# Optimization experiments

Measured on AMD Instinct MI355X. Metric: run time of the kernel, lower is better.

The kernel has to match this reference:

```python
import jax, jax.numpy as jnp
import numpy as np

B, C, K, V, S = 16384, 1024, 128, 256, 6
HM, HG, M = 512, 384, 1024
LB = 2
GATE_DIM = C + K + 2 * V + 5  # 1669
CADENCE = 8.0
TEMP = 0.25
REFRESH_T, SPAWN_T, PROMOTE_T, RETIRE_T = 0.55, 0.60, 0.50, 0.15
DECAY = 0.995
EPS_N = 1e-6


def _mlp(x, W1, b1, W2, b2):
    return jax.nn.gelu(x @ W1 + b1, approximate=False) @ W2 + b2


def _l2norm(x):
    n = jnp.linalg.norm(x, axis=-1, keepdims=True)
    return x / jnp.maximum(n, EPS_N)


def setup_inputs():
    key = jax.random.key(0)
    ks = jax.random.split(key, 16)
    p = lambda k, sh: (0.02 * jax.random.normal(k, sh)).astype(jnp.float32)
    return {
        "context": jax.random.normal(ks[0], (B, C), jnp.float32),
        "ledger_bias": jax.random.normal(ks[1], (B, LB), jnp.float32),
        "keys": jax.random.normal(ks[2], (B, S, K), jnp.float32),
        "values": jax.random.normal(ks[3], (B, S, V), jnp.float32),
        "confidence": jax.random.uniform(ks[4], (B, S, 1), jnp.float32),
        "age": 16.0 * jax.random.uniform(ks[5], (B, S, 1), jnp.float32),
        "alive": (jax.random.uniform(ks[6], (B, S, 1)) > 0.3).astype(jnp.float32),
        "Wk1": p(ks[7], (C, HM)), "bk1": jnp.zeros(HM, jnp.float32),
        "Wk2": p(ks[8], (HM, K)), "bk2": jnp.zeros(K, jnp.float32),
        "Wv1": p(ks[9], (C, HM)), "bv1": jnp.zeros(HM, jnp.float32),
        "Wv2": p(ks[10], (HM, V)), "bv2": jnp.zeros(V, jnp.float32),
        "Wg1": p(ks[11], (4, GATE_DIM, HG)), "bg1": jnp.zeros((4, HG), jnp.float32),
        "Wg2": p(ks[12], (4, HG, 1)), "bg2": jnp.zeros((4, 1), jnp.float32),
        "Wsum": p(ks[13], (V, M)), "bsum": jnp.zeros(M, jnp.float32),
        "g_ln": jnp.ones(M, jnp.float32), "b_ln": jnp.zeros(M, jnp.float32),
    }


def _forward(context, ledger_bias, keys, values, confidence, age, alive,
             Wk1, bk1, Wk2, bk2, Wv1, bv1, Wv2, bv2,
             Wg1, bg1, Wg2, bg2, Wsum, bsum, g_ln, b_ln):
    cand_key = _l2norm(_mlp(context, Wk1, bk1, Wk2, bk2))   # [B,K]
    cand_val = _mlp(context, Wv1, bv1, Wv2, bv2)            # [B,V]
    # --- slot match: cosine similarity over live slots, gather best ---
    live = alive[..., 0] > 0                                # [B,S]
    safe_keys = _l2norm(keys + (1.0 - alive) * 1e-4)
    scores = jnp.einsum("bd,bsd->bs", cand_key, safe_keys)
    scores = jnp.where(live, scores, -1e4)
    has_live = jnp.any(live, axis=1, keepdims=True)         # [B,1]
    best_score = jnp.where(has_live, scores.max(axis=1, keepdims=True), 0.0)
    best_index = jnp.where(has_live, jnp.argmax(scores, axis=1, keepdims=True), 0)
    matched_val = jnp.take_along_axis(values, best_index[:, :, None], axis=1)[:, 0]
    matched_age = jnp.take_along_axis(age, best_index[:, :, None], axis=1)[:, 0]
    cadence_prior = jax.nn.sigmoid((matched_age - CADENCE) / CADENCE)
    surprise = 1.0 - best_score
    feats = jnp.concatenate([context, cand_key, cand_val, matched_val,
                             best_score, cadence_prior, surprise, ledger_bias], axis=-1)
    # --- four gate MLPs fused into one batched einsum ---
    h = jax.nn.gelu(jnp.einsum("bf,gfh->bgh", feats, Wg1) + bg1, approximate=False)
    probs = jax.nn.sigmoid(jnp.einsum("bgh,gho->bgo", h, Wg2) + bg2)[:, :, 0]  # [B,4]
    refresh_p, spawn_p, promote_p, retire_p = (probs[:, i:i + 1] for i in range(4))
    # --- soft masks (hard=False path) ---
    has_live_f = alive.max(axis=1)                          # [B,1]
    t = max(TEMP, 1e-4)
    refresh_raw = jax.nn.sigmoid((refresh_p - REFRESH_T) / t) * has_live_f
    spawn_raw = jax.nn.sigmoid((spawn_p - SPAWN_T) / t)
    denom = 1.0 + refresh_raw + spawn_raw
    refresh = refresh_raw / denom
    spawn = spawn_raw / denom
    promote = jax.nn.sigmoid((promote_p - PROMOTE_T) / t)
    retire = jax.nn.sigmoid((retire_p - RETIRE_T) / t)
    # --- spawn slot selection ---
    inactive = (alive[..., 0] < 0.5).astype(jnp.float32)
    has_inactive = inactive.max(axis=1, keepdims=True) > 0.5
    inactive_choice = jnp.argmax(inactive, axis=1, keepdims=True)
    utility = (confidence - 0.01 * age)[..., 0]
    utility = jnp.where(best_index == jnp.arange(S)[None, :], 1e4, utility)
    spawn_index = jnp.where(has_inactive, inactive_choice,
                            jnp.argmin(utility, axis=1, keepdims=True))
    # --- masked scatter update into slot memory ---
    match_hot = jax.nn.one_hot(best_index[:, 0], S, dtype=keys.dtype)[:, :, None]
    spawn_hot = jax.nn.one_hot(spawn_index[:, 0], S, dtype=keys.dtype)[:, :, None]
    refresh_slot = match_hot * refresh[:, None, :]
    spawn_slot = spawn_hot * spawn[:, None, :]
    retire_slot = match_hot * retire[:, None, :]
    write = jnp.clip(refresh_slot + spawn_slot, 0.0, 1.0)
    keys_n = keys * (1.0 - write) + write * cand_key[:, None, :]
    values_n = values * (1.0 - write) + write * cand_val[:, None, :]
    conf_n = (confidence * DECAY * (1.0 - write) + write) * (1.0 - retire_slot)
    age_n = (age + alive) * (1.0 - write)
    alive_n = jnp.clip(alive * (1.0 - retire_slot) + write, 0.0, 1.0)
    # --- confidence-weighted summary + promoted memory token ---
    w = alive_n * conf_n
    summary = (values_n * w).sum(axis=1) / (w.sum(axis=1) + EPS_N)  # [B,V]
    z = summary @ Wsum + bsum
    mu = z.mean(axis=-1, keepdims=True)
    var = ((z - mu) ** 2).mean(axis=-1, keepdims=True)
    promoted = promote * (((z - mu) / jnp.sqrt(var + 1e-5)) * g_ln + b_ln)
    return promoted, summary, keys_n, values_n, conf_n, age_n, alive_n


def reference(context, ledger_bias, keys, values, confidence, age, alive,
              Wk1, bk1, Wk2, bk2, Wv1, bv1, Wv2, bv2,
              Wg1, bg1, Wg2, bg2, Wsum, bsum, g_ln, b_ln):
    return _forward(context, ledger_bias, keys, values, confidence, age, alive,
                    Wk1, bk1, Wk2, bk2, Wv1, bv1, Wv2, bv2,
                    Wg1, bg1, Wg2, bg2, Wsum, bsum, g_ln, b_ln)
```

## Files before the change

kernel.cpp:

```cpp
#include <hip/hip_runtime.h>
#include <math.h>

static constexpr int Bsz  = 16384;
static constexpr int Cdim = 1024;
static constexpr int Kdim = 128;
static constexpr int Vdim = 256;
static constexpr int HMd  = 512;
static constexpr int GOUTd= 1536;
static constexpr int GDIM = 1669;
static constexpr int GPAD = 1728;
static constexpr int F2D  = 704;
static constexpr int Mdim = 1024;
static constexpr float TAU = 2e-3f;

typedef __attribute__((ext_vector_type(8))) _Float16 f16x8;
typedef __attribute__((ext_vector_type(4))) _Float16 f16x4;
typedef __attribute__((ext_vector_type(4))) float f32x4;

__device__ __forceinline__ float sigm(float x){ return 1.0f/(1.0f+__expf(-x)); }
__device__ __forceinline__ float gelu(float x){
    float y = 0.70710678118654752440f * x;
    float a = fabsf(y);
    float t1 = __builtin_amdgcn_rcpf(fmaf(0.3275911f, a, 1.0f));
    float p = t1*fmaf(t1, fmaf(t1, fmaf(t1, fmaf(t1, 1.061405429f, -1.453152027f),
                                         1.421413741f), -0.284496736f), 0.254829592f);
    float e = __expf(-a*a);
    float er = fmaf(-p, e, 1.0f);
    er = (y < 0.0f) ? -er : er;
    return 0.5f*x*(1.0f+er);
}
__device__ __forceinline__ ushort f2h(float f){
    return __builtin_bit_cast(ushort, (_Float16)f);
}
__device__ __forceinline__ unsigned f2q4(float a, float b, float c, float d){
    int v = 0;
    v = __builtin_amdgcn_cvt_pk_fp8_f32(a, b, v, false);
    v = __builtin_amdgcn_cvt_pk_fp8_f32(c, d, v, true);
    return (unsigned)v;
}


__global__ __launch_bounds__(256) void k_zero(int* p){ if (threadIdx.x==0) *p = 0; }

__global__ __launch_bounds__(256) void k_cat(float* __restrict__ dst,
        const float* __restrict__ a, const float* __restrict__ b, int na, int ntot){
    int i = blockIdx.x*256 + threadIdx.x;
    if (i >= ntot) return;
    dst[i] = (i < na) ? a[i] : b[i-na];
}

__global__ __launch_bounds__(256) void k_wt(const float* __restrict__ W,
                                            ushort* __restrict__ Wt, int K, int N){
    __shared__ float tile[64][65];
    int n0 = blockIdx.x*64, k0 = blockIdx.y*64;
    int tx = threadIdx.x & 63, ty = threadIdx.x >> 6;
    #pragma unroll
    for (int i=0;i<64;i+=4)
        tile[ty+i][tx] = W[(size_t)(k0+ty+i)*N + n0 + tx];
    __syncthreads();
    #pragma unroll
    for (int i=0;i<64;i+=4)
        Wt[(size_t)(n0+ty+i)*K + k0 + tx] = f2h(tile[tx][ty+i]);
}

__global__ __launch_bounds__(256) void k_wg1t8(const float* __restrict__ Wg1,
                                               unsigned char* __restrict__ B8){
    __shared__ float tile[64][65];
    int g  = blockIdx.z;
    int h0 = blockIdx.x*64;
    int f0 = blockIdx.y*64;
    int tx = threadIdx.x & 63, ty = threadIdx.x >> 6;
    #pragma unroll
    for (int i=0;i<64;i+=4)
        tile[ty+i][tx] = Wg1[((size_t)g*GDIM + f0+ty+i)*384 + h0+tx];
    __syncthreads();
    int u = threadIdx.x & 7, nl0 = threadIdx.x >> 3;
    #pragma unroll
    for (int i=0;i<2;i++){
        int nl = nl0 + i*32;
        float v[8];
        #pragma unroll
        for (int j=0;j<8;j++) v[j] = tile[u*8+j][nl];
        unsigned q0 = f2q4(v[0],v[1],v[2],v[3]), q1 = f2q4(v[4],v[5],v[6],v[7]);
        int n  = g*384 + h0 + nl;
        int ur = (f0>>3) + u;
        int seg = ur >> 4, ul = ur & 15;
        size_t pos = (size_t)n*1024 + seg*128 + (size_t)(ul ^ (n&7))*8;
        ((unsigned*)(B8+pos))[0] = q0;
        ((unsigned*)(B8+pos))[1] = q1;
    }
}

__global__ __launch_bounds__(256) void k_wg1tf(const float* __restrict__ Wg1,
                                               ushort* __restrict__ Wt){
    __shared__ float tile[64][65];
    int g  = blockIdx.z;
    int h0 = blockIdx.x*64;
    int k0 = blockIdx.y*64;
    int tx = threadIdx.x & 63, ty = threadIdx.x >> 6;
    #pragma unroll
    for (int i=0;i<64;i+=4){
        int f = 1024 + k0 + ty + i;
        tile[ty+i][tx] = (f < GDIM) ? Wg1[((size_t)g*GDIM + f)*384 + h0+tx] : 0.0f;
    }
    __syncthreads();
    #pragma unroll
    for (int i=0;i<64;i+=4)
        Wt[((size_t)(g*384 + h0+ty+i))*F2D + k0 + tx] = f2h(tile[tx][ty+i]);
}

__global__ __launch_bounds__(256) void k_cvt8(const float* __restrict__ x,
        ushort* __restrict__ yh, unsigned char* __restrict__ y8, int nunits){
    int i = blockIdx.x*256 + threadIdx.x;
    if (i >= nunits) return;
    const float4* src = (const float4*)(x + (size_t)i*8);
    float4 v0 = src[0], v1 = src[1];
    ushort4 h0 = { f2h(v0.x), f2h(v0.y), f2h(v0.z), f2h(v0.w) };
    ushort4 h1 = { f2h(v1.x), f2h(v1.y), f2h(v1.z), f2h(v1.w) };
    ((ushort4*)yh)[(size_t)i*2]   = h0;
    ((ushort4*)yh)[(size_t)i*2+1] = h1;
    unsigned q0 = f2q4(v0.x,v0.y,v0.z,v0.w), q1 = f2q4(v1.x,v1.y,v1.z,v1.w);
    int row = i >> 7;
    int ur  = i & 127;
    int seg = ur >> 4, ul = ur & 15;
    size_t pos = (size_t)row*1024 + seg*128 + (size_t)(ul ^ (row&7))*8;
    ((unsigned*)(y8+pos))[0] = q0;
    ((unsigned*)(y8+pos))[1] = q1;
}

__device__ __forceinline__ void gload_lds16(const void* g, void* l){
    typedef __attribute__((address_space(1))) const unsigned gu32;
    typedef __attribute__((address_space(3))) unsigned lu32;
    __builtin_amdgcn_global_load_lds((gu32*)(unsigned long long)g,
                                     (lu32*)(unsigned)(unsigned long long)l,
                                     16, 0, 0);
}

template<int ACT, int OUTM, int SRC, int NX>
__global__ __launch_bounds__(512, 4) void k_mgemm(const ushort* __restrict__ A,
        const ushort* __restrict__ A2, const ushort* __restrict__ Bt,
        const float* __restrict__ bias, const float* __restrict__ Wg2,
        void* __restrict__ Cout, int K, int lda){
    __shared__ alignas(16) ushort lds[24576];
    ushort* As = lds;
    ushort* Bs = lds + 16384;
    int t = threadIdx.x;
    int l = t & 63, wv = t >> 6;
    int wrow = wv >> 1, wcol = wv & 1;
    int nwg = NX * (int)gridDim.y;
    int orig = (int)blockIdx.y * NX + (int)blockIdx.x;
    int qq = nwg >> 3, rr = nwg & 7;
    int xcd = orig & 7, loc = orig >> 3;
    int wgid = (xcd < rr ? xcd*(qq+1) : rr*(qq+1) + (xcd-rr)*qq) + loc;
    int bx = wgid % NX;
    int by = wgid / NX;
    size_t row0 = (size_t)by * 256;
    int col0 = bx * 128;
    constexpr int N = NX*128;
    f32x4 acc[4][4] = {};
    int lrow = l >> 3;
    int lc8  = (l & 7) ^ lrow;

    for (int k0 = 0; k0 < K; k0 += 64){
        const ushort* Ag; size_t astr; int koff;
        if (SRC == 2){
            Ag = A; astr = (size_t)lda; koff = k0 + (bx ? 512 : 0);
        } else { Ag = A; astr = (size_t)lda; koff = k0; }
        #pragma unroll
        for (int i = 0; i < 4; ++i){
            int ch = wv*4 + i;
            int r  = ch*8 + lrow;
            gload_lds16(Ag + (row0 + r)*astr + koff + lc8*8, As + ch*512);
        }
        #pragma unroll
        for (int i = 0; i < 2; ++i){
            int ch = wv*2 + i;
            int r  = ch*8 + lrow;
            gload_lds16(Bt + (size_t)(col0 + r)*K + k0 + lc8*8, Bs + ch*512);
        }
        __syncthreads();
        #pragma unroll
        for (int kk = 0; kk < 2; ++kk){
            f16x8 af[4], bfr[4];
            int j8 = kk*4 + (l >> 4);
            #pragma unroll
            for (int m = 0; m < 4; ++m){
                int row = wrow*64 + m*16 + (l & 15);
                int c16 = j8 ^ (row & 7);
                af[m] = *(const f16x8*)(const void*)(As + row*64 + c16*8);
            }
            #pragma unroll
            for (int n = 0; n < 4; ++n){
                int rowb = wcol*64 + n*16 + (l & 15);
                int c16 = j8 ^ (rowb & 7);
                bfr[n] = *(const f16x8*)(const void*)(Bs + rowb*64 + c16*8);
            }
            #pragma unroll
            for (int m = 0; m < 4; ++m)
                #pragma unroll
                for (int n = 0; n < 4; ++n)
                    acc[m][n] = __builtin_amdgcn_mfma_f32_16x16x32_f16(af[m], bfr[n], acc[m][n], 0, 0, 0);
        }
        __syncthreads();
    }
    int q = l >> 4, cf = l & 15;
    #pragma unroll
    for (int m = 0; m < 4; ++m){
        #pragma unroll
        for (int n = 0; n < 4; ++n){
            int col = col0 + wcol*64 + n*16 + cf;
            float bv = bias[col];
            #pragma unroll
            for (int i = 0; i < 4; ++i){
                size_t r = row0 + wrow*64 + m*16 + q*4 + i;
                float v = acc[m][n][i] + bv;
                if (ACT == 1) v = gelu(v);
                if (OUTM == 1) ((ushort*)Cout)[r*N + col] = f2h(v);
                else           ((float*) Cout)[r*N + col] = v;
            }
        }
    }
}

__global__ __launch_bounds__(512, 4) void k_ggemm(const unsigned char* __restrict__ A8,
        const ushort* __restrict__ Af, const unsigned char* __restrict__ B8,
        const ushort* __restrict__ Bf, const float* __restrict__ bias,
        const float* __restrict__ Wg2, float* __restrict__ part){
    __shared__ alignas(16) unsigned char lds[49152];
    unsigned char* As8 = lds;
    unsigned char* Bs8 = lds + 32768;
    ushort* As16 = (ushort*)lds;
    ushort* Bs16 = (ushort*)(lds + 32768);
    int t = threadIdx.x, l = t & 63, wv = t >> 6;
    int wrow = wv >> 1, wcol = wv & 1;
    constexpr int NX = 12;
    int nwg = NX * (int)gridDim.y;
    int orig = (int)blockIdx.y * NX + (int)blockIdx.x;
    int qq = nwg >> 3, rr = nwg & 7;
    int xcd = orig & 7, loc = orig >> 3;
    int wgid = (xcd < rr ? xcd*(qq+1) : rr*(qq+1) + (xcd-rr)*qq) + loc;
    int bx = wgid % NX;
    int by = wgid / NX;
    size_t row0 = (size_t)by * 256;
    int col0 = bx * 128;
    f32x4 acc[4][4] = {};
    int lrow = l >> 3;

    for (int kt = 0; kt < 8; ++kt){
        int k0 = kt << 7;
        #pragma unroll
        for (int i = 0; i < 4; ++i){
            int ch = wv*4 + i;
            int r  = ch*8 + lrow;
            gload_lds16(A8 + (row0 + r)*1024 + k0 + (l&7)*16, As8 + ch*1024);
        }
        #pragma unroll
        for (int i = 0; i < 2; ++i){
            int ch = wv*2 + i;
            int r  = ch*8 + lrow;
            gload_lds16(B8 + (size_t)(col0 + r)*1024 + k0 + (l&7)*16, Bs8 + ch*1024);
        }
        __syncthreads();
        #pragma unroll
        for (int kk = 0; kk < 4; ++kk){
            long a8[4], b8[4];
            int j8 = (l >> 4) + kk*4;
            #pragma unroll
            for (int m = 0; m < 4; ++m){
                int row = wrow*64 + m*16 + (l & 15);
                int u = j8 ^ (row & 7);
                a8[m] = *(const long*)(const void*)(As8 + row*128 + u*8);
            }
            #pragma unroll
            for (int n = 0; n < 4; ++n){
                int col = wcol*64 + n*16 + (l & 15);
                int u = j8 ^ (col & 7);
                b8[n] = *(const long*)(const void*)(Bs8 + col*128 + u*8);
            }
            #pragma unroll
            for (int m = 0; m < 4; ++m)
                #pragma unroll
                for (int n = 0; n < 4; ++n)
                    acc[m][n] = __builtin_amdgcn_mfma_f32_16x16x32_fp8_fp8(a8[m], b8[n], acc[m][n], 0, 0, 0);
        }
        __syncthreads();
    }
    int lc8 = (l & 7) ^ lrow;
    for (int tt = 0; tt < 11; ++tt){
        int k0 = tt << 6;
        #pragma unroll
        for (int i = 0; i < 4; ++i){
            int ch = wv*4 + i;
            int r  = ch*8 + lrow;
            gload_lds16(Af + (row0 + r)*(size_t)F2D + k0 + lc8*8, As16 + ch*512);
        }
        #pragma unroll
        for (int i = 0; i < 2; ++i){
            int ch = wv*2 + i;
            int r  = ch*8 + lrow;
            gload_lds16(Bf + (size_t)(col0 + r)*F2D + k0 + lc8*8, Bs16 + ch*512);
        }
        __syncthreads();
        #pragma unroll
        for (int kk = 0; kk < 2; ++kk){
            f16x8 af[4], bfr[4];
            int j8 = kk*4 + (l >> 4);
            #pragma unroll
            for (int m = 0; m < 4; ++m){
                int row = wrow*64 + m*16 + (l & 15);
                int c16 = j8 ^ (row & 7);
                af[m] = *(const f16x8*)(const void*)(As16 + row*64 + c16*8);
            }
            #pragma unroll
            for (int n = 0; n < 4; ++n){
                int col = wcol*64 + n*16 + (l & 15);
                int c16 = j8 ^ (col & 7);
                bfr[n] = *(const f16x8*)(const void*)(Bs16 + col*64 + c16*8);
            }
            #pragma unroll
            for (int m = 0; m < 4; ++m)
                #pragma unroll
                for (int n = 0; n < 4; ++n)
                    acc[m][n] = __builtin_amdgcn_mfma_f32_16x16x32_f16(af[m], bfr[n], acc[m][n], 0, 0, 0);
        }
        __syncthreads();
    }
    int q = l >> 4, cf = l & 15;
    float* sacc = (float*)lds;
    if (t < 256) sacc[t] = 0.f;
    __syncthreads();
    #pragma unroll
    for (int m = 0; m < 4; ++m){
        #pragma unroll
        for (int i = 0; i < 4; ++i){
            float v = 0.f;
            #pragma unroll
            for (int n = 0; n < 4; ++n){
                int col = col0 + wcol*64 + n*16 + cf;
                float z = acc[m][n][i] + bias[col];
                v += gelu(z) * Wg2[col];
            }
            atomicAdd(&sacc[wrow*64 + m*16 + q*4 + i], v);
        }
    }
    __syncthreads();
    if (t < 256) part[(row0 + t)*NX + bx] = sacc[t];
}

template<int ACT, int GATHER>
__global__ __launch_bounds__(256) void k_gemm_dyn(const float* __restrict__ A,
                                                  const float* __restrict__ W,
                                                  const float* __restrict__ bias,
                                                  float* __restrict__ C,
                                                  const int* __restrict__ cntp,
                                                  const int* __restrict__ flaglist,
                                                  int b0, int N, int K){
    int cnt = *cntp;
    int M = (cnt + 63) & ~63;
    size_t row0 = (size_t)blockIdx.y * 64;
    if ((int)row0 >= M) return;
    __shared__ float As[32][68];
    __shared__ float Ws[32][64];
    int t  = threadIdx.x;
    int tx = t & 15, ty = t >> 4;
    int col0 = blockIdx.x * 64;
    float acc[4][4] = {};
    int ra = t >> 3;
    int ca = (t & 7) << 2;
    int rw = t >> 4;
    int cw = (t & 15) << 2;
    const float *Arow0, *Arow1;
    if (GATHER){
        int r1 = (int)row0 + ra, r2 = r1 + 32;
        int f1 = (r1 < cnt) ? flaglist[r1] : 0;
        int f2 = (r2 < cnt) ? flaglist[r2] : 0;
        Arow0 = A + ((size_t)b0 + f1)*K;
        Arow1 = A + ((size_t)b0 + f2)*K;
    } else {
        Arow0 = A + (row0 + ra)*(size_t)K;
        Arow1 = A + (row0 + ra + 32)*(size_t)K;
    }
    for (int k0 = 0; k0 < K; k0 += 32){
        float4 a0 = *(const float4*)(Arow0 + k0 + ca);
        float4 a1 = *(const float4*)(Arow1 + k0 + ca);
        float4 w0 = *(const float4*)(W + (size_t)(k0 + rw)*N + col0 + cw);
        float4 w1 = *(const float4*)(W + (size_t)(k0 + rw + 16)*N + col0 + cw);
        As[ca+0][ra] = a0.x; As[ca+1][ra] = a0.y; As[ca+2][ra] = a0.z; As[ca+3][ra] = a0.w;
        As[ca+0][ra+32] = a1.x; As[ca+1][ra+32] = a1.y; As[ca+2][ra+32] = a1.z; As[ca+3][ra+32] = a1.w;
        *(float4*)&Ws[rw][cw]    = w0;
        *(float4*)&Ws[rw+16][cw] = w1;
        __syncthreads();
        #pragma unroll
        for (int kk = 0; kk < 32; ++kk){
            float4 av = *(const float4*)&As[kk][ty*4];
            float4 wv = *(const float4*)&Ws[kk][tx*4];
            float a4[4] = {av.x, av.y, av.z, av.w};
            float w4[4] = {wv.x, wv.y, wv.z, wv.w};
            #pragma unroll
            for (int i=0;i<4;i++)
                #pragma unroll
                for (int j=0;j<4;j++)
                    acc[i][j] = fmaf(a4[i], w4[j], acc[i][j]);
        }
        __syncthreads();
    }
    #pragma unroll
    for (int i=0;i<4;i++){
        size_t r = row0 + ty*4 + i;
        #pragma unroll
        for (int j=0;j<4;j++){
            int c = col0 + tx*4 + j;
            float v = acc[i][j] + bias[c];
            if (ACT == 1) v = gelu(v);
            C[r*N + c] = v;
        }
    }
}

__global__ __launch_bounds__(256) void k_fixapply(const float* __restrict__ fck,
        const float* __restrict__ keys, const float* __restrict__ values,
        const float* __restrict__ age,  const float* __restrict__ alive,
        float* __restrict__ ckc, ushort* __restrict__ feats2, int* __restrict__ bidx,
        const int* __restrict__ flagcnt, const int* __restrict__ flaglist, int b0){
    int i = (blockIdx.x<<2) + (threadIdx.x>>6);
    int lane = threadIdx.x & 63;
    if (i >= *flagcnt) return;
    int w = flaglist[i];
    size_t b = (size_t)b0 + w;
    float2 c2 = ((const float2*)(fck + (size_t)i*128))[lane];
    float ss = c2.x*c2.x + c2.y*c2.y;
    #pragma unroll
    for (int o=32;o;o>>=1) ss += __shfl_xor(ss,o);
    float inv = 1.0f / fmaxf(sqrtf(ss), 1e-6f);
    float2 cc; cc.x = c2.x*inv; cc.y = c2.y*inv;
    ((float2*)(ckc + (size_t)w*128))[lane] = cc;
    ushort* f2 = feats2 + (size_t)w*F2D;
    { ushort2 o = { f2h(cc.x), f2h(cc.y) };
      ((ushort2*)f2)[lane] = o; }
    float s1v = -1e30f; int bi = 0; int anylive = 0;
    #pragma unroll
    for (int s=0;s<6;s++){
        float a = alive[b*6+s];
        float2 k2 = ((const float2*)(keys + (b*6+s)*128))[lane];
        float ks = k2.x*k2.x + k2.y*k2.y;
        float dt = cc.x*k2.x + cc.y*k2.y;
        #pragma unroll
        for (int o=32;o;o>>=1){ ks += __shfl_xor(ks,o); dt += __shfl_xor(dt,o); }
        float sc;
        if (a > 0.0f){ sc = dt / fmaxf(sqrtf(ks), 1e-6f); anylive = 1; }
        else sc = -1e4f;
        if (sc > s1v){ s1v = sc; bi = s; }
    }
    int bis = anylive ? bi : 0;
    float bsc = anylive ? s1v : 0.0f;
    float4 mv = ((const float4*)(values + (b*6+bis)*256))[lane];
    ushort4 mo = { f2h(mv.x), f2h(mv.y), f2h(mv.z), f2h(mv.w) };
    ((ushort4*)(f2+384))[lane] = mo;
    if (lane == 0){
        bidx[w] = bis;
        float mage = age[b*6 + bis];
        f2[640] = f2h(bsc);
        f2[641] = f2h(sigm((mage - 8.0f)*0.125f));
        f2[642] = f2h(1.0f - bsc);
    }
}

__global__ __launch_bounds__(256) void k_feats(
        const float* __restrict__ ledger, const float* __restrict__ keys,
        const float* __restrict__ values, const float* __restrict__ age,
        const float* __restrict__ alive,  const float* __restrict__ ckv,
        float* __restrict__ ckc, ushort* __restrict__ feats2,
        int* __restrict__ bidx, int* __restrict__ flagcnt, int* __restrict__ flaglist,
        int b0){
    int w = (blockIdx.x<<2) + (threadIdx.x>>6);
    int lane = threadIdx.x & 63;
    size_t b = (size_t)b0 + w;
    const float* ckr = ckv + (size_t)w*384;
    float2 cr2 = ((const float2*)ckr)[lane];
    float ssc = cr2.x*cr2.x + cr2.y*cr2.y;
    #pragma unroll
    for (int o=32;o;o>>=1) ssc += __shfl_xor(ssc,o);
    float invc = 1.0f / fmaxf(sqrtf(ssc), 1e-6f);
    float2 cc; cc.x = cr2.x*invc; cc.y = cr2.y*invc;
    ((float2*)(ckc + (size_t)w*128))[lane] = cc;
    float s1v = -1e30f, s2v = -1e30f; int bi = 0; int anylive = 0;
    #pragma unroll
    for (int s=0;s<6;s++){
        float a = alive[b*6+s];
        float2 k2 = ((const float2*)(keys + (b*6+s)*128))[lane];
        float ss = k2.x*k2.x + k2.y*k2.y;
        float dt = cc.x*k2.x + cc.y*k2.y;
        #pragma unroll
        for (int o=32;o;o>>=1){ ss += __shfl_xor(ss,o); dt += __shfl_xor(dt,o); }
        float sc;
        if (a > 0.0f){ sc = dt / fmaxf(sqrtf(ss), 1e-6f); anylive = 1; }
        else sc = -1e4f;
        if (sc > s1v){ s2v = s1v; s1v = sc; bi = s; }
        else if (sc > s2v) s2v = sc;
    }
    float best_score = anylive ? s1v : 0.0f;
    int bis = anylive ? bi : 0;
    if (lane == 0 && (s1v - s2v) < TAU){
        int pos = atomicAdd(flagcnt, 1);
        flaglist[pos] = w;
    }
    float4 mv = ((const float4*)(values + (b*6+bis)*256))[lane];
    float mage = age[b*6+bis];
    float cad = sigm((mage - 8.0f)*0.125f);
    ushort* f2 = feats2 + (size_t)w*F2D;
    { ushort2 o = { f2h(cc.x), f2h(cc.y) };
      ((ushort2*)f2)[lane] = o; }
    { float4 v = ((const float4*)(ckr+128))[lane];
      ushort4 o = { f2h(v.x), f2h(v.y), f2h(v.z), f2h(v.w) };
      ((ushort4*)(f2+128))[lane] = o; }
    { ushort4 o = { f2h(mv.x), f2h(mv.y), f2h(mv.z), f2h(mv.w) };
      ((ushort4*)(f2+384))[lane] = o; }
    if (lane == 0){
        f2[640] = f2h(best_score);
        f2[641] = f2h(cad);
        f2[642] = f2h(1.0f - best_score);
        f2[643] = f2h(ledger[b*2]);
        f2[644] = f2h(ledger[b*2+1]);
        bidx[w] = bis;
    }
    if (lane < GPAD - GDIM) f2[645+lane] = 0;
}

__global__ __launch_bounds__(256) void k_update(const float* __restrict__ keys,
        const float* __restrict__ values, const float* __restrict__ conf,
        const float* __restrict__ age,    const float* __restrict__ alive,
        const float* __restrict__ ckC,    const float* __restrict__ ckv,
        const float* __restrict__ part,   const float* __restrict__ bg2,
        const int* __restrict__ bidx,
        float* __restrict__ probsC,
        float* __restrict__ o_keys, float* __restrict__ o_vals,
        float* __restrict__ o_conf, float* __restrict__ o_age,
        float* __restrict__ o_aliv, float* __restrict__ o_sum,
        ushort* __restrict__ o_sumb, int b0){
    int w = (blockIdx.x<<2) + (threadIdx.x>>6);
    int lane = threadIdx.x & 63;
    size_t b = (size_t)b0 + w;
    const float* pp = part + (size_t)w*12;
    float pb[4];
    #pragma unroll
    for (int g=0; g<4; ++g)
        pb[g] = sigm(pp[3*g] + pp[3*g+1] + pp[3*g+2] + bg2[g]);
    if (lane < 4) probsC[w*4 + lane] = pb[lane];
    float rp = pb[0], sp = pb[1], tp = pb[3];
    float al[6], cf[6], ag[6];
    float hl = 0.f;
    #pragma unroll
    for (int s=0;s<6;s++){
        al[s]=alive[b*6+s]; cf[s]=conf[b*6+s]; ag[s]=age[b*6+s];
        hl = fmaxf(hl, al[s]);
    }
    float rr = hl * sigm((rp-0.55f)*4.0f);
    float sr = sigm((sp-0.60f)*4.0f);
    float den = 1.0f + rr + sr;
    float refresh = rr/den, spawn = sr/den;
    float retire = sigm((tp-0.15f)*4.0f);
    int bi = bidx[w];
    int ic = -1;
    #pragma unroll
    for (int s=5;s>=0;s--) if (al[s] < 0.5f) ic = s;
    int si;
    if (ic >= 0) si = ic;
    else {
        float bu = 1e30f; int am = 0;
        #pragma unroll
        for (int s=0;s<6;s++){
            float u = (s == bi) ? 1e4f : (cf[s] - 0.01f*ag[s]);
            if (u < bu){ bu = u; am = s; }
        }
        si = am;
    }
    float2 cc  = ((const float2*)(ckC + (size_t)w*128))[lane];
    float4 cvv = ((const float4*)(ckv + (size_t)w*384 + 128))[lane];
    float s0=0,s1=0,s2=0,s3=0, wsum=0;
    #pragma unroll
    for (int s=0;s<6;s++){
        float wr = refresh*(s==bi ? 1.0f:0.0f) + spawn*(s==si ? 1.0f:0.0f);
        wr = fminf(wr, 1.0f);
        float rs = (s==bi) ? retire : 0.0f;
        float om = 1.0f - wr;
        float2 k2 = ((const float2*)(keys + (b*6+s)*128))[lane];
        float2 kn; kn.x = k2.x*om + wr*cc.x; kn.y = k2.y*om + wr*cc.y;
        ((float2*)(o_keys + (b*6+s)*128))[lane] = kn;
        float4 vv = ((const float4*)(values + (b*6+s)*256))[lane];
        float4 vn;
        vn.x = vv.x*om + wr*cvv.x; vn.y = vv.y*om + wr*cvv.y;
        vn.z = vv.z*om + wr*cvv.z; vn.w = vv.w*om + wr*cvv.w;
        ((float4*)(o_vals + (b*6+s)*256))[lane] = vn;
        float cn  = (cf[s]*0.995f*om + wr) * (1.0f - rs);
        float an  = fminf(fmaxf(al[s]*(1.0f - rs) + wr, 0.0f), 1.0f);
        float agn = (ag[s] + al[s]) * om;
        float wgt = an * cn;
        wsum += wgt;
        s0 += vn.x*wgt; s1 += vn.y*wgt; s2 += vn.z*wgt; s3 += vn.w*wgt;
        if (lane == s){ o_conf[b*6+s] = cn; o_age[b*6+s] = agn; o_aliv[b*6+s] = an; }
    }
    float inv = 1.0f/(wsum + 1e-6f);
    float4 sm; sm.x = s0*inv; sm.y = s1*inv; sm.z = s2*inv; sm.w = s3*inv;
    ((float4*)(o_sum + b*256))[lane] = sm;
    ushort4 sb = { f2h(sm.x), f2h(sm.y), f2h(sm.z), f2h(sm.w) };
    ((ushort4*)(o_sumb + (size_t)w*256))[lane] = sb;
}

__global__ __launch_bounds__(256) void k_ln(const ushort* __restrict__ z,
        const float* __restrict__ probs, const float* __restrict__ g_ln,
        const float* __restrict__ b_ln,  float* __restrict__ o_prom, int b0){
    int w = blockIdx.x; int t = threadIdx.x;
    int lane = t & 63, wid = t >> 6;
    f16x4 hv = ((const f16x4*)(z + (size_t)w*1024))[t];
    float v0 = (float)hv[0], v1 = (float)hv[1], v2 = (float)hv[2], v3 = (float)hv[3];
    float s = v0+v1+v2+v3;
    #pragma unroll
    for (int o=32;o;o>>=1) s += __shfl_xor(s,o);
    __shared__ float red[4];
    if (lane==0) red[wid] = s;
    __syncthreads();
    float mu = (red[0]+red[1]+red[2]+red[3]) * (1.0f/1024.0f);
    float d0=v0-mu, d1=v1-mu, d2=v2-mu, d3=v3-mu;
    float ss = d0*d0+d1*d1+d2*d2+d3*d3;
    #pragma unroll
    for (int o=32;o;o>>=1) ss += __shfl_xor(ss,o);
    __syncthreads();
    if (lane==0) red[wid] = ss;
    __syncthreads();
    float var = (red[0]+red[1]+red[2]+red[3]) * (1.0f/1024.0f);
    float rstd = 1.0f / sqrtf(var + 1e-5f);
    float pm = sigm((probs[w*4+2]-0.50f)*4.0f);
    float4 g  = ((const float4*)g_ln)[t];
    float4 bb = ((const float4*)b_ln)[t];
    float4 o;
    o.x = pm*(d0*rstd*g.x + bb.x);
    o.y = pm*(d1*rstd*g.y + bb.y);
    o.z = pm*(d2*rstd*g.z + bb.z);
    o.w = pm*(d3*rstd*g.w + bb.w);
    ((float4*)(o_prom + ((size_t)b0 + w)*1024))[t] = o;
}

extern "C" void kernel_launch(void* const* d_in, const int* in_sizes, int n_in,
                              void* d_out, int out_size, void* d_ws, size_t ws_size,
                              hipStream_t stream){
    const float* ctx    = (const float*)d_in[0];
    const float* ledger = (const float*)d_in[1];
    const float* keys   = (const float*)d_in[2];
    const float* values = (const float*)d_in[3];
    const float* conf   = (const float*)d_in[4];
    const float* age    = (const float*)d_in[5];
    const float* alive  = (const float*)d_in[6];
    const float* Wk1 = (const float*)d_in[7];  const float* bk1 = (const float*)d_in[8];
    const float* Wk2 = (const float*)d_in[9];  const float* bk2 = (const float*)d_in[10];
    const float* Wv1 = (const float*)d_in[11]; const float* bv1 = (const float*)d_in[12];
    const float* Wv2 = (const float*)d_in[13]; const float* bv2 = (const float*)d_in[14];
    const float* Wg1 = (const float*)d_in[15]; const float* bg1 = (const float*)d_in[16];
    const float* Wg2 = (const float*)d_in[17]; const float* bg2 = (const float*)d_in[18];
    const float* Wsum= (const float*)d_in[19]; const float* bsum= (const float*)d_in[20];
    const float* g_ln= (const float*)d_in[21]; const float* b_ln= (const float*)d_in[22];

    float* out   = (float*)d_out;
    float* o_prom= out;
    float* o_sum = o_prom + (size_t)Bsz*Mdim;
    float* o_keys= o_sum  + (size_t)Bsz*Vdim;
    float* o_vals= o_keys + (size_t)Bsz*6*Kdim;
    float* o_conf= o_vals + (size_t)Bsz*6*Vdim;
    float* o_age = o_conf + (size_t)Bsz*6;
    float* o_aliv= o_age  + (size_t)Bsz*6;

    char* p = (char*)d_ws;
    auto alloc = [&](size_t bytes)->char*{
        char* r = p; p += (bytes + 255) & ~(size_t)255; return r;
    };
    ushort* ctxh  = (ushort*)alloc((size_t)Bsz*Cdim*2);
    unsigned char* ctx8 = (unsigned char*)alloc((size_t)Bsz*Cdim);
    ushort* W1m   = (ushort*)alloc((size_t)1024*Cdim*2);
    ushort* W2m   = (ushort*)alloc((size_t)384*HMd*2);
    unsigned char* Wg1t8 = (unsigned char*)alloc((size_t)GOUTd*1024);
    ushort* Wg1tf = (ushort*)alloc((size_t)GOUTd*F2D*2);
    ushort* Wsumt = (ushort*)alloc((size_t)Mdim*Vdim*2);
    float*  biasm1= (float*) alloc(1024*4);
    float*  biasm2= (float*) alloc(384*4);
    size_t fixed = (size_t)(p - (char*)d_ws);
    size_t per_row = 2048 + 1536 + 512 + 1408 + 48 + 4096 + 512 + 16
                   + 4 + 4 + 2048 + 512 + 128;
    int CB = 16384;
    while (CB > 256 && fixed + (size_t)CB*per_row + 16384 > ws_size) CB >>= 1;
    ushort* H      = (ushort*)alloc((size_t)CB*1024*2);
    float*  ckv    = (float*) alloc((size_t)CB*384*4);
    float*  ckc    = (float*) alloc((size_t)CB*Kdim*4);
    ushort* feats2 = (ushort*)alloc((size_t)CB*F2D*2);
    float*  part   = (float*) alloc((size_t)CB*12*4);
    float*  zbuf   = (float*) alloc((size_t)CB*Mdim*4);
    ushort* sumb   = (ushort*)alloc((size_t)CB*Vdim*2);
    float*  probsC = (float*) alloc((size_t)CB*4*4);
    int*    bidxC  = (int*)   alloc((size_t)CB*4);
    int*    flagl  = (int*)   alloc((size_t)CB*4);
    int*    flagc  = (int*)   alloc(256);
    float*  fH     = (float*) alloc((size_t)CB*HMd*4);
    float*  fck    = (float*) alloc((size_t)CB*Kdim*4);
    ushort* zh     = (ushort*)zbuf;

    dim3 blk(256);
    dim3 blk512(512);
    k_cvt8<<<(int)(((size_t)Bsz*Cdim/8 + 255)/256), blk, 0, stream>>>(
        ctx, ctxh, ctx8, (int)((size_t)Bsz*Cdim/8));
    k_wt<<<dim3(HMd/64,  Cdim/64), blk, 0, stream>>>(Wk1, W1m,             Cdim, HMd);
    k_wt<<<dim3(HMd/64,  Cdim/64), blk, 0, stream>>>(Wv1, W1m + 512*Cdim,  Cdim, HMd);
    k_wt<<<dim3(Kdim/64, HMd/64),  blk, 0, stream>>>(Wk2, W2m,             HMd, Kdim);
    k_wt<<<dim3(Vdim/64, HMd/64),  blk, 0, stream>>>(Wv2, W2m + 128*HMd,   HMd, Vdim);
    k_wt<<<dim3(Mdim/64, Vdim/64), blk, 0, stream>>>(Wsum, Wsumt, Vdim, Mdim);
    k_wg1t8<<<dim3(6, 16, 4), blk, 0, stream>>>(Wg1, Wg1t8);
    k_wg1tf<<<dim3(6, 11, 4), blk, 0, stream>>>(Wg1, Wg1tf);
    k_cat<<<(1024+255)/256, blk, 0, stream>>>(biasm1, bk1, bv1, 512, 1024);
    k_cat<<<(384+255)/256,  blk, 0, stream>>>(biasm2, bk2, bv2, 128, 384);

    for (int b0 = 0; b0 < Bsz; b0 += CB){
        k_zero<<<1, blk, 0, stream>>>(flagc);
        k_mgemm<1,1,0,8><<<dim3(8, CB/256), blk512, 0, stream>>>(
            ctxh + (size_t)b0*Cdim, nullptr, W1m, biasm1, nullptr, H, Cdim, Cdim);
        k_mgemm<0,0,2,3><<<dim3(3, CB/256), blk512, 0, stream>>>(
            H, nullptr, W2m, biasm2, nullptr, ckv, HMd, 1024);
        k_feats<<<CB/4, blk, 0, stream>>>(ledger, keys, values, age, alive,
                                          ckv, ckc, feats2, bidxC, flagc, flagl, b0);
        k_gemm_dyn<1,1><<<dim3(HMd/64,  CB/64), blk, 0, stream>>>(
            ctx, Wk1, bk1, fH, flagc, flagl, b0, HMd, Cdim);
        k_gemm_dyn<0,0><<<dim3(Kdim/64, CB/64), blk, 0, stream>>>(
            fH, Wk2, bk2, fck, flagc, nullptr, 0, Kdim, HMd);
        k_fixapply<<<CB/4, blk, 0, stream>>>(fck, keys, values, age, alive,
                                             ckc, feats2, bidxC, flagc, flagl, b0);
        k_ggemm<<<dim3(12, CB/256), blk512, 0, stream>>>(
            ctx8 + (size_t)b0*Cdim, feats2, Wg1t8, Wg1tf, bg1, Wg2, part);
        k_update<<<CB/4, blk, 0, stream>>>(keys, values, conf, age, alive, ckc, ckv,
                                           part, bg2, bidxC, probsC,
                                           o_keys, o_vals, o_conf, o_age, o_aliv,
                                           o_sum, sumb, b0);
        k_mgemm<0,1,0,8><<<dim3(8, CB/256), blk512, 0, stream>>>(
            sumb, nullptr, Wsumt, bsum, nullptr, zh, Vdim, Vdim);
        k_ln<<<CB, blk, 0, stream>>>(zh, probsC, g_ln, b_ln, o_prom, b0);
    }
}
```

Measured before the change: 444.3 us.

## Quantize gate feature tail to FP8 and fold into single FP8 GEMM loop

The gate GEMM's second phase, which multiplied the 704-wide feature tail in FP16 MFMA, is replaced by FP8. A new kernel converts the FP16 features to swizzled FP8 rows, and the weight tail is pre-quantized the same way, so one 14-step FP8 loop covers both the context and the feature parts. Separately, the dynamic fixup GEMMs now use a fixed grid of 16 row blocks that stride over the flagged rows instead of launching CB/64 blocks that mostly exit early. This trades an extra conversion pass and lower precision on the gate features for halved operand bytes and faster MFMA in the tail.

New measurement: 455.9 us. +2.6%, slower.

```diff
diff --git a/kernel.cpp b/kernel.cpp
--- a/kernel.cpp
+++ b/kernel.cpp
@@ -8,8 +8,9 @@
 static constexpr int HMd  = 512;
 static constexpr int GOUTd= 1536;
 static constexpr int GDIM = 1669;
-static constexpr int GPAD = 1728;
+static constexpr int GPAD = 1792;
 static constexpr int F2D  = 704;
+static constexpr int F8D  = 768;
 static constexpr int Mdim = 1024;
 static constexpr float TAU = 2e-3f;
 
@@ -91,8 +92,8 @@
     }
 }
 
-__global__ __launch_bounds__(256) void k_wg1tf(const float* __restrict__ Wg1,
-                                               ushort* __restrict__ Wt){
+__global__ __launch_bounds__(256) void k_wg1tf8(const float* __restrict__ Wg1,
+                                                unsigned char* __restrict__ B8){
     __shared__ float tile[64][65];
     int g  = blockIdx.z;
     int h0 = blockIdx.x*64;
@@ -104,9 +105,21 @@
         tile[ty+i][tx] = (f < GDIM) ? Wg1[((size_t)g*GDIM + f)*384 + h0+tx] : 0.0f;
     }
     __syncthreads();
-    #pragma unroll
-    for (int i=0;i<64;i+=4)
-        Wt[((size_t)(g*384 + h0+ty+i))*F2D + k0 + tx] = f2h(tile[tx][ty+i]);
+    int u = threadIdx.x & 7, nl0 = threadIdx.x >> 3;
+    #pragma unroll
+    for (int i=0;i<2;i++){
+        int nl = nl0 + i*32;
+        float v[8];
+        #pragma unroll
+        for (int j=0;j<8;j++) v[j] = tile[u*8+j][nl];
+        unsigned q0 = f2q4(v[0],v[1],v[2],v[3]), q1 = f2q4(v[4],v[5],v[6],v[7]);
+        int n  = g*384 + h0 + nl;
+        int ur = (k0>>3) + u;
+        int seg = ur >> 4, ul = ur & 15;
+        size_t pos = (size_t)n*F8D + seg*128 + (size_t)(ul ^ (n&7))*8;
+        ((unsigned*)(B8+pos))[0] = q0;
+        ((unsigned*)(B8+pos))[1] = q1;
+    }
 }
 
 __global__ __launch_bounds__(256) void k_cvt8(const float* __restrict__ x,
@@ -126,6 +139,25 @@
     size_t pos = (size_t)row*1024 + seg*128 + (size_t)(ul ^ (row&7))*8;
     ((unsigned*)(y8+pos))[0] = q0;
     ((unsigned*)(y8+pos))[1] = q1;
+}
+
+__global__ __launch_bounds__(256) void k_f2q8(const ushort* __restrict__ f16,
+        unsigned char* __restrict__ f8, int total){
+    int idx = blockIdx.x*256 + threadIdx.x;
+    if (idx >= total) return;
+    int w = idx / 96, ur = idx - w*96;
+    int c0 = ur*8;
+    float v[8];
+    #pragma unroll
+    for (int j=0;j<8;j++){
+        int c = c0+j;
+        v[j] = (c < F2D) ? (float)(*(const _Float16*)&f16[(size_t)w*F2D + c]) : 0.0f;
+    }
+    unsigned q0 = f2q4(v[0],v[1],v[2],v[3]), q1 = f2q4(v[4],v[5],v[6],v[7]);
+    int seg = ur >> 4, ul = ur & 15;
+    size_t pos = (size_t)w*F8D + seg*128 + (size_t)(ul ^ (w&7))*8;
+    ((unsigned*)(f8+pos))[0] = q0;
+    ((unsigned*)(f8+pos))[1] = q1;
 }
 
 __device__ __forceinline__ void gload_lds16(const void* g, void* l){
@@ -223,14 +255,12 @@
 }
 
 __global__ __launch_bounds__(512, 4) void k_ggemm(const unsigned char* __restrict__ A8,
-        const ushort* __restrict__ Af, const unsigned char* __restrict__ B8,
-        const ushort* __restrict__ Bf, const float* __restrict__ bias,
+        const unsigned char* __restrict__ F8, const unsigned char* __restrict__ B8,
+        const unsigned char* __restrict__ BF8, const float* __restrict__ bias,
         const float* __restrict__ Wg2, float* __restrict__ part){
     __shared__ alignas(16) unsigned char lds[49152];
     unsigned char* As8 = lds;
     unsigned char* Bs8 = lds + 32768;
-    ushort* As16 = (ushort*)lds;
-    ushort* Bs16 = (ushort*)(lds + 32768);
     int t = threadIdx.x, l = t & 63, wv = t >> 6;
     int wrow = wv >> 1, wcol = wv & 1;
     constexpr int NX = 12;
@@ -246,24 +276,26 @@
     f32x4 acc[4][4] = {};
     int lrow = l >> 3;
 
-    for (int kt = 0; kt < 8; ++kt){
-        int k0 = kt << 7;
+    for (int kt = 0; kt < 14; ++kt){
+        const unsigned char *Ab, *Bb; size_t astr; int koff;
+        if (kt < 8){ Ab = A8; Bb = B8;  astr = 1024; koff = kt << 7; }
+        else       { Ab = F8; Bb = BF8; astr = F8D;  koff = (kt-8) << 7; }
         #pragma unroll
         for (int i = 0; i < 4; ++i){
             int ch = wv*4 + i;
             int r  = ch*8 + lrow;
-            gload_lds16(A8 + (row0 + r)*1024 + k0 + (l&7)*16, As8 + ch*1024);
+            gload_lds16(Ab + (row0 + r)*astr + koff + (l&7)*16, As8 + ch*1024);
         }
         #pragma unroll
         for (int i = 0; i < 2; ++i){
             int ch = wv*2 + i;
             int r  = ch*8 + lrow;
-            gload_lds16(B8 + (size_t)(col0 + r)*1024 + k0 + (l&7)*16, Bs8 + ch*1024);
+            gload_lds16(Bb + (size_t)(col0 + r)*astr + koff + (l&7)*16, Bs8 + ch*1024);
         }
         __syncthreads();
         #pragma unroll
         for (int kk = 0; kk < 4; ++kk){
-            long a8[4], b8[4];
+            long a8[4], b8v[4];
             int j8 = (l >> 4) + kk*4;
             #pragma unroll
             for (int m = 0; m < 4; ++m){
@@ -275,53 +307,13 @@
             for (int n = 0; n < 4; ++n){
                 int col = wcol*64 + n*16 + (l & 15);
                 int u = j8 ^ (col & 7);
-                b8[n] = *(const long*)(const void*)(Bs8 + col*128 + u*8);
+                b8v[n] = *(const long*)(const void*)(Bs8 + col*128 + u*8);
             }
             #pragma unroll
             for (int m = 0; m < 4; ++m)
                 #pragma unroll
                 for (int n = 0; n < 4; ++n)
-                    acc[m][n] = __builtin_amdgcn_mfma_f32_16x16x32_fp8_fp8(a8[m], b8[n], acc[m][n], 0, 0, 0);
-        }
-        __syncthreads();
-    }
-    int lc8 = (l & 7) ^ lrow;
-    for (int tt = 0; tt < 11; ++tt){
-        int k0 = tt << 6;
-        #pragma unroll
-        for (int i = 0; i < 4; ++i){
-            int ch = wv*4 + i;
-            int r  = ch*8 + lrow;
-            gload_lds16(Af + (row0 + r)*(size_t)F2D + k0 + lc8*8, As16 + ch*512);
-        }
-        #pragma unroll
-        for (int i = 0; i < 2; ++i){
-            int ch = wv*2 + i;
-            int r  = ch*8 + lrow;
-            gload_lds16(Bf + (size_t)(col0 + r)*F2D + k0 + lc8*8, Bs16 + ch*512);
-        }
-        __syncthreads();
-        #pragma unroll
-        for (int kk = 0; kk < 2; ++kk){
-            f16x8 af[4], bfr[4];
-            int j8 = kk*4 + (l >> 4);
-            #pragma unroll
-            for (int m = 0; m < 4; ++m){
-                int row = wrow*64 + m*16 + (l & 15);
-                int c16 = j8 ^ (row & 7);
-                af[m] = *(const f16x8*)(const void*)(As16 + row*64 + c16*8);
-            }
-            #pragma unroll
-            for (int n = 0; n < 4; ++n){
-                int col = wcol*64 + n*16 + (l & 15);
-                int c16 = j8 ^ (col & 7);
-                bfr[n] = *(const f16x8*)(const void*)(Bs16 + col*64 + c16*8);
-            }
-            #pragma unroll
-            for (int m = 0; m < 4; ++m)
-                #pragma unroll
-                for (int n = 0; n < 4; ++n)
-                    acc[m][n] = __builtin_amdgcn_mfma_f32_16x16x32_f16(af[m], bfr[n], acc[m][n], 0, 0, 0);
+                    acc[m][n] = __builtin_amdgcn_mfma_f32_16x16x32_fp8_fp8(a8[m], b8v[n], acc[m][n], 0, 0, 0);
         }
         __syncthreads();
     }
@@ -357,62 +349,62 @@
                                                   int b0, int N, int K){
     int cnt = *cntp;
     int M = (cnt + 63) & ~63;
-    size_t row0 = (size_t)blockIdx.y * 64;
-    if ((int)row0 >= M) return;
     __shared__ float As[32][68];
     __shared__ float Ws[32][64];
     int t  = threadIdx.x;
     int tx = t & 15, ty = t >> 4;
     int col0 = blockIdx.x * 64;
-    float acc[4][4] = {};
     int ra = t >> 3;
     int ca = (t & 7) << 2;
     int rw = t >> 4;
     int cw = (t & 15) << 2;
-    const float *Arow0, *Arow1;
-    if (GATHER){
-        int r1 = (int)row0 + ra, r2 = r1 + 32;
-        int f1 = (r1 < cnt) ? flaglist[r1] : 0;
-        int f2 = (r2 < cnt) ? flaglist[r2] : 0;
-        Arow0 = A + ((size_t)b0 + f1)*K;
-        Arow1 = A + ((size_t)b0 + f2)*K;
-    } else {
-        Arow0 = A + (row0 + ra)*(size_t)K;
-        Arow1 = A + (row0 + ra + 32)*(size_t)K;
-    }
-    for (int k0 = 0; k0 < K; k0 += 32){
-        float4 a0 = *(const float4*)(Arow0 + k0 + ca);
-        float4 a1 = *(const float4*)(Arow1 + k0 + ca);
-        float4 w0 = *(const float4*)(W + (size_t)(k0 + rw)*N + col0 + cw);
-        float4 w1 = *(const float4*)(W + (size_t)(k0 + rw + 16)*N + col0 + cw);
-        As[ca+0][ra] = a0.x; As[ca+1][ra] = a0.y; As[ca+2][ra] = a0.z; As[ca+3][ra] = a0.w;
-        As[ca+0][ra+32] = a1.x; As[ca+1][ra+32] = a1.y; As[ca+2][ra+32] = a1.z; As[ca+3][ra+32] = a1.w;
-        *(float4*)&Ws[rw][cw]    = w0;
-        *(float4*)&Ws[rw+16][cw] = w1;
-        __syncthreads();
-        #pragma unroll
-        for (int kk = 0; kk < 32; ++kk){
-            float4 av = *(const float4*)&As[kk][ty*4];
-            float4 wv = *(const float4*)&Ws[kk][tx*4];
-            float a4[4] = {av.x, av.y, av.z, av.w};
-            float w4[4] = {wv.x, wv.y, wv.z, wv.w};
-            #pragma unroll
-            for (int i=0;i<4;i++)
+    for (int row0 = (int)blockIdx.y*64; row0 < M; row0 += (int)gridDim.y*64){
+        float acc[4][4] = {};
+        const float *Arow0, *Arow1;
+        if (GATHER){
+            int r1 = row0 + ra, r2 = r1 + 32;
+            int f1 = (r1 < cnt) ? flaglist[r1] : 0;
+            int f2 = (r2 < cnt) ? flaglist[r2] : 0;
+            Arow0 = A + ((size_t)b0 + f1)*K;
+            Arow1 = A + ((size_t)b0 + f2)*K;
+        } else {
+            Arow0 = A + (size_t)(row0 + ra)*K;
+            Arow1 = A + (size_t)(row0 + ra + 32)*K;
+        }
+        for (int k0 = 0; k0 < K; k0 += 32){
+            float4 a0 = *(const float4*)(Arow0 + k0 + ca);
+            float4 a1 = *(const float4*)(Arow1 + k0 + ca);
+            float4 w0 = *(const float4*)(W + (size_t)(k0 + rw)*N + col0 + cw);
+            float4 w1 = *(const float4*)(W + (size_t)(k0 + rw + 16)*N + col0 + cw);
+            As[ca+0][ra] = a0.x; As[ca+1][ra] = a0.y; As[ca+2][ra] = a0.z; As[ca+3][ra] = a0.w;
+            As[ca+0][ra+32] = a1.x; As[ca+1][ra+32] = a1.y; As[ca+2][ra+32] = a1.z; As[ca+3][ra+32] = a1.w;
+            *(float4*)&Ws[rw][cw]    = w0;
+            *(float4*)&Ws[rw+16][cw] = w1;
+            __syncthreads();
+            #pragma unroll
+            for (int kk = 0; kk < 32; ++kk){
+                float4 av = *(const float4*)&As[kk][ty*4];
+                float4 wv = *(const float4*)&Ws[kk][tx*4];
+                float a4[4] = {av.x, av.y, av.z, av.w};
+                float w4[4] = {wv.x, wv.y, wv.z, wv.w};
                 #pragma unroll
-                for (int j=0;j<4;j++)
-                    acc[i][j] = fmaf(a4[i], w4[j], acc[i][j]);
-        }
-        __syncthreads();
-    }
-    #pragma unroll
-    for (int i=0;i<4;i++){
-        size_t r = row0 + ty*4 + i;
-        #pragma unroll
-        for (int j=0;j<4;j++){
-            int c = col0 + tx*4 + j;
-            float v = acc[i][j] + bias[c];
-            if (ACT == 1) v = gelu(v);
-            C[r*N + c] = v;
+                for (int i=0;i<4;i++)
+                    #pragma unroll
+                    for (int j=0;j<4;j++)
+                        acc[i][j] = fmaf(a4[i], w4[j], acc[i][j]);
+            }
+            __syncthreads();
+        }
+        #pragma unroll
+        for (int i=0;i<4;i++){
+            size_t r = (size_t)row0 + ty*4 + i;
+            #pragma unroll
+            for (int j=0;j<4;j++){
+                int c = col0 + tx*4 + j;
+                float v = acc[i][j] + bias[c];
+                if (ACT == 1) v = gelu(v);
+                C[r*N + c] = v;
+            }
         }
     }
 }
@@ -523,7 +515,7 @@
         f2[644] = f2h(ledger[b*2+1]);
         bidx[w] = bis;
     }
-    if (lane < GPAD - GDIM) f2[645+lane] = 0;
+    if (lane < F2D - 645) f2[645+lane] = 0;
 }
 
 __global__ __launch_bounds__(256) void k_update(const float* __restrict__ keys,
@@ -676,20 +668,21 @@
     unsigned char* ctx8 = (unsigned char*)alloc((size_t)Bsz*Cdim);
     ushort* W1m   = (ushort*)alloc((size_t)1024*Cdim*2);
     ushort* W2m   = (ushort*)alloc((size_t)384*HMd*2);
-    unsigned char* Wg1t8 = (unsigned char*)alloc((size_t)GOUTd*1024);
-    ushort* Wg1tf = (ushort*)alloc((size_t)GOUTd*F2D*2);
+    unsigned char* Wg1t8  = (unsigned char*)alloc((size_t)GOUTd*1024);
+    unsigned char* Wg1tf8 = (unsigned char*)alloc((size_t)GOUTd*F8D);
     ushort* Wsumt = (ushort*)alloc((size_t)Mdim*Vdim*2);
     float*  biasm1= (float*) alloc(1024*4);
     float*  biasm2= (float*) alloc(384*4);
     size_t fixed = (size_t)(p - (char*)d_ws);
-    size_t per_row = 2048 + 1536 + 512 + 1408 + 48 + 4096 + 512 + 16
-                   + 4 + 4 + 2048 + 512 + 128;
+    size_t per_row = 2048 + 1536 + 512 + 1408 + 768 + 48 + 4096 + 512 + 16
+                   + 4 + 4 + 2048 + 512 + 160;
     int CB = 16384;
     while (CB > 256 && fixed + (size_t)CB*per_row + 16384 > ws_size) CB >>= 1;
     ushort* H      = (ushort*)alloc((size_t)CB*1024*2);
     float*  ckv    = (float*) alloc((size_t)CB*384*4);
     float*  ckc    = (float*) alloc((size_t)CB*Kdim*4);
     ushort* feats2 = (ushort*)alloc((size_t)CB*F2D*2);
+    unsigned char* feats8 = (unsigned char*)alloc((size_t)CB*F8D);
     float*  part   = (float*) alloc((size_t)CB*12*4);
     float*  zbuf   = (float*) alloc((size_t)CB*Mdim*4);
     ushort* sumb   = (ushort*)alloc((size_t)CB*Vdim*2);
@@ -711,7 +704,7 @@
     k_wt<<<dim3(Vdim/64, HMd/64),  blk, 0, stream>>>(Wv2, W2m + 128*HMd,   HMd, Vdim);
     k_wt<<<dim3(Mdim/64, Vdim/64), blk, 0, stream>>>(Wsum, Wsumt, Vdim, Mdim);
     k_wg1t8<<<dim3(6, 16, 4), blk, 0, stream>>>(Wg1, Wg1t8);
-    k_wg1tf<<<dim3(6, 11, 4), blk, 0, stream>>>(Wg1, Wg1tf);
+    k_wg1tf8<<<dim3(6, 12, 4), blk, 0, stream>>>(Wg1, Wg1tf8);
     k_cat<<<(1024+255)/256, blk, 0, stream>>>(biasm1, bk1, bv1, 512, 1024);
     k_cat<<<(384+255)/256,  blk, 0, stream>>>(biasm2, bk2, bv2, 128, 384);
 
@@ -723,14 +716,15 @@
             H, nullptr, W2m, biasm2, nullptr, ckv, HMd, 1024);
         k_feats<<<CB/4, blk, 0, stream>>>(ledger, keys, values, age, alive,
                                           ckv, ckc, feats2, bidxC, flagc, flagl, b0);
-        k_gemm_dyn<1,1><<<dim3(HMd/64,  CB/64), blk, 0, stream>>>(
+        k_gemm_dyn<1,1><<<dim3(HMd/64, 16), blk, 0, stream>>>(
             ctx, Wk1, bk1, fH, flagc, flagl, b0, HMd, Cdim);
-        k_gemm_dyn<0,0><<<dim3(Kdim/64, CB/64), blk, 0, stream>>>(
+        k_gemm_dyn<0,0><<<dim3(Kdim/64, 16), blk, 0, stream>>>(
             fH, Wk2, bk2, fck, flagc, nullptr, 0, Kdim, HMd);
         k_fixapply<<<CB/4, blk, 0, stream>>>(fck, keys, values, age, alive,
                                              ckc, feats2, bidxC, flagc, flagl, b0);
+        k_f2q8<<<(CB*96 + 255)/256, blk, 0, stream>>>(feats2, feats8, CB*96);
         k_ggemm<<<dim3(12, CB/256), blk512, 0, stream>>>(
-            ctx8 + (size_t)b0*Cdim, feats2, Wg1t8, Wg1tf, bg1, Wg2, part);
+            ctx8 + (size_t)b0*Cdim, feats8, Wg1t8, Wg1tf8, bg1, Wg2, part);
         k_update<<<CB/4, blk, 0, stream>>>(keys, values, conf, age, alive, ckc, ckv,
                                            part, bg2, bidxC, probsC,
                                            o_keys, o_vals, o_conf, o_age, o_aliv,
```
